# Kernel tuning notes

Measured on AMD Instinct MI355X. Metric: run time of the kernel, lower is better.

Reference implementation:

```python
import jax, jax.numpy as jnp
import numpy as np

N_EMBD = 1024
HEAD_SIZE = 64

def setup_inputs() -> dict:
    key = jax.random.key(0)
    kx, kk, kq, kv = jax.random.split(key, 4)
    x = jax.random.normal(kx, (8, 2048, N_EMBD), dtype=jnp.float32)
    # torch nn.Linear(n_embd, head_size, bias=False): y = x @ W.T, W:[head_size,n_embd].
    # We store the transposed form [n_embd, head_size] directly.
    s = 1.0 / np.sqrt(N_EMBD)
    Wk = jax.random.uniform(kk, (N_EMBD, HEAD_SIZE), jnp.float32, -s, s)
    Wq = jax.random.uniform(kq, (N_EMBD, HEAD_SIZE), jnp.float32, -s, s)
    Wv = jax.random.uniform(kv, (N_EMBD, HEAD_SIZE), jnp.float32, -s, s)
    return {"x": x, "Wk": Wk, "Wq": Wq, "Wv": Wv}

def reference(x, Wk, Wq, Wv):
    B, T, C = x.shape
    k = jnp.einsum('btc,cd->btd', x, Wk)  # [B,T,d]
    q = jnp.einsum('btc,cd->btd', x, Wq)
    v = jnp.einsum('btc,cd->btd', x, Wv)
    d = k.shape[-1]
    wei = jnp.einsum('btd,bsd->bts', q, k) * (d ** -0.5)  # [B,T,T]
    causal = jnp.tril(jnp.ones((T, T), dtype=bool))
    wei = jnp.where(causal, wei, -jnp.inf)
    wei = jax.nn.softmax(wei, axis=-1)
    # dropout p=0.0 -> identity (eval-mode equivalent)
    out = jnp.einsum('bts,bsd->btd', wei, v)  # [B,T,d]
    return out
```

## Files before the change

### kernel.cpp

```cpp
#include <hip/hip_runtime.h>
#include <hip/hip_bf16.h>

#define TB 8
#define TT 2048
#define TC 1024
#define TD 64
#define PSP 72

typedef __attribute__((ext_vector_type(8))) short bf16x8;
typedef __attribute__((ext_vector_type(4))) float f32x4;

__device__ __forceinline__ short f2bf(float f) {
    union { float f; unsigned u; } v; v.f = f;
    unsigned r = v.u + 0x7fffu + ((v.u >> 16) & 1u);
    return (short)(r >> 16);
}

__device__ __forceinline__ unsigned pk2(float a, float b) {
    __hip_bfloat162 h = __float22bfloat162_rn(make_float2(a, b));
    union { __hip_bfloat162 h2; unsigned u; } c; c.h2 = h;
    return c.u;
}

__device__ __forceinline__ void gl_lds16(const void* g, void* l) {
    __builtin_amdgcn_global_load_lds(
        (const __attribute__((address_space(1))) unsigned*)g,
        (__attribute__((address_space(3))) unsigned*)l, 16, 0, 0);
}

__device__ __forceinline__ void bar_raw() { asm volatile("s_barrier" ::: "memory"); }
#define WAIT_VM(n) asm volatile("s_waitcnt vmcnt(" #n ")" ::: "memory")

__global__ __launch_bounds__(256) void convert_w(const float* __restrict__ Wk,
                                                 const float* __restrict__ Wq,
                                                 const float* __restrict__ Wv,
                                                 short* __restrict__ Wt) {
    __shared__ short Tl[64 * PSP];
    const int tid = threadIdx.x;
    const int kc  = blockIdx.x;
    const int oid = blockIdx.y;
    const float* src = (oid == 0) ? Wk : (oid == 1) ? Wq : Wv;
    const float scale = (oid == 1) ? 0.125f : 1.0f;
    const int row = tid >> 2;
    const int c0  = (tid & 3) << 4;

    const float* sp = src + (size_t)(kc * 64 + row) * TD + c0;
    float4 a = ((const float4*)sp)[0], b = ((const float4*)sp)[1];
    float4 c = ((const float4*)sp)[2], d = ((const float4*)sp)[3];
    float vals[16] = {a.x,a.y,a.z,a.w, b.x,b.y,b.z,b.w,
                      c.x,c.y,c.z,c.w, d.x,d.y,d.z,d.w};
#pragma unroll
    for (int j = 0; j < 16; ++j)
        Tl[(c0 + j) * PSP + row] = f2bf(vals[j] * scale);
    __syncthreads();

    const int n  = tid >> 2;
    const int k0 = (tid & 3) << 4;
    uint4 u0 = *(uint4*)&Tl[n * PSP + k0];
    uint4 u1 = *(uint4*)&Tl[n * PSP + k0 + 8];
    uint4* dst = (uint4*)(Wt + (size_t)(oid * 64 + n) * TC + kc * 64 + k0);
    dst[0] = u0; dst[1] = u1;
}

__global__ __launch_bounds__(256, 1) void qkv_proj(const float* __restrict__ x,
                                                   const short* __restrict__ Wt,
                                                   short* __restrict__ qb,
                                                   short* __restrict__ kb,
                                                   short* __restrict__ vt) {
    __shared__ __align__(16) char sm[3 * 40960];
    const int tid = threadIdx.x;
    const int mg  = blockIdx.x;
    const int wv  = tid >> 6, lane = tid & 63;
    const int wu  = __builtin_amdgcn_readfirstlane(wv);
    const int l15 = lane & 15, quad = lane >> 4;
    const int mh  = wv >> 1;
    const int nh  = wv & 1;

    f32x4 acc[2][6];
#pragma unroll
    for (int i = 0; i < 2; ++i)
#pragma unroll
        for (int j = 0; j < 6; ++j) acc[i][j] = (f32x4){0.f, 0.f, 0.f, 0.f};

    const float* xtile = x + (size_t)mg * 64 * TC;

#define STAGE_Q(r)                                                          \
    {                                                                       \
        char* sb = sm + ((r) % 3) * 40960;                                  \
        float* xd = (float*)sb;                                             \
        short* wd = (short*)(sb + 16384);                                   \
        _Pragma("unroll")                                                   \
        for (int j = 0; j < 4; ++j) {                                       \
            int sbase = (j * 4 + wu) * 64;                                  \
            int sl = sbase + lane;                                          \
            int rw = sl >> 4, g = sl & 15;                                  \
            int gg = g ^ (rw & 15);                                         \
            gl_lds16(xtile + (size_t)rw * TC + (r) * 64 + gg * 4,           \
                     xd + (size_t)sbase * 4);                               \
        }                                                                   \
        _Pragma("unroll")                                                   \
        for (int j = 0; j < 6; ++j) {                                       \
            int n0 = (j * 4 + wu) * 8;                                      \
            int nb = n0 + (lane >> 3), g = lane & 7;                        \
            int gg = g ^ (nb & 7);                                          \
            gl_lds16(Wt + (size_t)nb * TC + (r) * 64 + gg * 8,              \
                     wd + (size_t)n0 * 64);                                 \
        }                                                                   \
    }

    STAGE_Q(0);
    STAGE_Q(1);
    for (int r = 0; r < 16; ++r) {
        if (r + 2 < 16)      { STAGE_Q(r + 2); WAIT_VM(20); }
        else if (r + 1 < 16) { WAIT_VM(10); }
        else                 { WAIT_VM(0); }
        bar_raw();
        const char* sb = sm + (r % 3) * 40960;
        const float* xb = (const float*)sb;
        const short* wb = (const short*)(sb + 16384);
#pragma unroll
        for (int c = 0; c < 2; ++c) {
            int G = c * 8 + quad * 2;
#pragma unroll
            for (int mt = 0; mt < 2; ++mt) {
                const int xrow = (mh * 32 + mt * 16 + l15) * 16;
                float4 f0 = *(const float4*)(xb + (xrow + (G ^ l15)) * 4);
                float4 f1 = *(const float4*)(xb + (xrow + ((G + 1) ^ l15)) * 4);
                union { bf16x8 v; unsigned u[4]; } pk;
                pk.u[0] = pk2(f0.x, f0.y); pk.u[1] = pk2(f0.z, f0.w);
                pk.u[2] = pk2(f1.x, f1.y); pk.u[3] = pk2(f1.z, f1.w);
#pragma unroll
                for (int i = 0; i < 6; ++i) {
                    int nt = nh * 6 + i;
                    bf16x8 B = *(const bf16x8*)(wb + (nt * 16 + l15) * 64
                                                + (((c * 4 + quad) ^ (l15 & 7)) * 8));
                    acc[mt][i] = __builtin_amdgcn_mfma_f32_16x16x32_bf16(
                                     pk.v, B, acc[mt][i], 0, 0, 0);
                }
            }
        }
        bar_raw();
    }
#undef STAGE_Q

    const int row0 = mg * 64 + mh * 32;
    const int bb = mg >> 5;
#pragma unroll
    for (int i = 0; i < 6; ++i) {
        int nt = nh * 6 + i;
        if (nt < 4) {
#pragma unroll
            for (int mt = 0; mt < 2; ++mt)
#pragma unroll
                for (int rr = 0; rr < 4; ++rr)
                    kb[(size_t)(row0 + mt * 16 + quad * 4 + rr) * TD + nt * 16 + l15]
                        = f2bf(acc[mt][rr >> 2 ? 0 : i][rr]);
        }
    }
#pragma unroll
    for (int i = 0; i < 6; ++i) {
        int nt = nh * 6 + i;
#pragma unroll
        for (int mt = 0; mt < 2; ++mt) {
            if (nt < 4) {
#pragma unroll
                for (int rr = 0; rr < 4; ++rr)
                    kb[(size_t)(row0 + mt * 16 + quad * 4 + rr) * TD + nt * 16 + l15]
                        = f2bf(acc[mt][i][rr]);
            } else if (nt < 8) {
#pragma unroll
                for (int rr = 0; rr < 4; ++rr)
                    qb[(size_t)(row0 + mt * 16 + quad * 4 + rr) * TD + (nt - 4) * 16 + l15]
                        = f2bf(acc[mt][i][rr]);
            } else {
                int d = (nt - 8) * 16 + l15;
                alignas(8) short t4[4];
#pragma unroll
                for (int rr = 0; rr < 4; ++rr) t4[rr] = f2bf(acc[mt][i][rr]);
                *(uint2*)(vt + (size_t)(bb * TD + d) * TT
                          + ((row0 + mt * 16) & 2047) + quad * 4) = *(uint2*)t4;
            }
        }
    }
}

__global__ __launch_bounds__(256, 2) void attn(const short* __restrict__ qb,
                                               const short* __restrict__ kb,
                                               const short* __restrict__ vt,
                                               float* __restrict__ out) {
    __shared__ __align__(16) char smem[58368];
    short* Ps = (short*)(smem + 49152);

    const int tid = threadIdx.x;
    const int pm  = blockIdx.x;
    const int b   = pm & 7;
    const int it  = 31 - (pm >> 3);
    const int wv  = tid >> 6, lane = tid & 63;
    const int wu  = __builtin_amdgcn_readfirstlane(wv);
    const int l15 = lane & 15, quad = lane >> 4;
    const int q0  = it * 64;
    const int KT  = it + 1;
    const float L2E = 1.4426950408889634f;

    const short* kbb = kb + (size_t)b * TT * TD;
    const short* vbb = vt + (size_t)b * TD * TT;
    short* myPs = Ps + wu * (16 * PSP);

    const size_t qoff = (size_t)(b * TT + q0 + wv * 16 + l15) * TD + quad * 8;
    bf16x8 aq0 = *(const bf16x8*)(qb + qoff);
    bf16x8 aq1 = *(const bf16x8*)(qb + qoff + 32);
    WAIT_VM(0);

    f32x4 O[4];
#pragma unroll
    for (int i = 0; i < 4; ++i) O[i] = (f32x4){0.f, 0.f, 0.f, 0.f};
    float lsum[4] = {0.f, 0.f, 0.f, 0.f};

#define STAGE_KV(r)                                                         \
    {                                                                       \
        char* sb = smem + ((r) % 3) * 16384;                                \
        short* kd = (short*)sb;                                             \
        short* vd = (short*)(sb + 8192);                                    \
        _Pragma("unroll")                                                   \
        for (int j = 0; j < 2; ++j) {                                       \
            int sbase = (j * 4 + wu) * 64;                                  \
            int sl = sbase + lane;                                          \
            int rw = sl >> 3, g = sl & 7;                                   \
            int gg = g ^ (rw & 7);                                          \
            gl_lds16(kbb + (size_t)((r) * 64 + rw) * TD + gg * 8,           \
                     kd + sbase * 8);                                       \
            gl_lds16(vbb + (size_t)rw * TT + (r) * 64 + gg * 8,             \
                     vd + sbase * 8);                                       \
        }                                                                   \
    }

    STAGE_KV(0);
    if (KT > 1) STAGE_KV(1);
    for (int r = 0; r < KT; ++r) {
        if (r + 2 < KT)      { STAGE_KV(r + 2); WAIT_VM(8); }
        else if (r + 1 < KT) { WAIT_VM(4); }
        else                 { WAIT_VM(0); }
        bar_raw();

        const char* sb2 = (const char*)smem + (r % 3) * 16384;
        const short* Kt = (const short*)sb2;
        const short* Vt = (const short*)(sb2 + 8192);
        f32x4 S[4];
#pragma unroll
        for (int nt = 0; nt < 4; ++nt) {
            int rw = nt * 16 + l15, r7 = l15 & 7;
            bf16x8 b0 = *(const bf16x8*)(Kt + rw * 64 + (quad ^ r7) * 8);
            bf16x8 b1 = *(const bf16x8*)(Kt + rw * 64 + ((4 + quad) ^ r7) * 8);
            S[nt] = (f32x4){0.f, 0.f, 0.f, 0.f};
            S[nt] = __builtin_amdgcn_mfma_f32_16x16x32_bf16(aq0, b0, S[nt], 0, 0, 0);
            S[nt] = __builtin_amdgcn_mfma_f32_16x16x32_bf16(aq1, b1, S[nt], 0, 0, 0);
        }
        const bool diag = (r == KT - 1);
        const int qrow = q0 + wv * 16 + quad * 4;
#pragma unroll
        for (int nt = 0; nt < 4; ++nt) {
            int scol = r * 64 + nt * 16 + l15;
#pragma unroll
            for (int r4 = 0; r4 < 4; ++r4) {
                float pv = exp2f(S[nt][r4] * L2E);
                if (diag && (scol > qrow + r4)) pv = 0.f;
                lsum[r4] += pv;
                myPs[(quad * 4 + r4) * PSP + nt * 16 + l15] = f2bf(pv);
            }
        }
        bf16x8 p0 = *(const bf16x8*)(myPs + l15 * PSP + quad * 8);
        bf16x8 p1 = *(const bf16x8*)(myPs + l15 * PSP + quad * 8 + 32);
#pragma unroll
        for (int dt = 0; dt < 4; ++dt) {
            int rw = dt * 16 + l15, r7 = l15 & 7;
            bf16x8 b0 = *(const bf16x8*)(Vt + rw * 64 + (quad ^ r7) * 8);
            bf16x8 b1 = *(const bf16x8*)(Vt + rw * 64 + ((4 + quad) ^ r7) * 8);
            O[dt] = __builtin_amdgcn_mfma_f32_16x16x32_bf16(p0, b0, O[dt], 0, 0, 0);
            O[dt] = __builtin_amdgcn_mfma_f32_16x16x32_bf16(p1, b1, O[dt], 0, 0, 0);
        }
        bar_raw();
    }
#undef STAGE_KV

#pragma unroll
    for (int r4 = 0; r4 < 4; ++r4) {
        float v = lsum[r4];
        v += __shfl_xor(v, 1); v += __shfl_xor(v, 2);
        v += __shfl_xor(v, 4); v += __shfl_xor(v, 8);
        lsum[r4] = v;
    }
#pragma unroll
    for (int dt = 0; dt < 4; ++dt)
#pragma unroll
        for (int r4 = 0; r4 < 4; ++r4)
            out[(size_t)(b * TT + q0 + wv * 16 + quad * 4 + r4) * TD + dt * 16 + l15]
                = O[dt][r4] / lsum[r4];
}

extern "C" void kernel_launch(void* const* d_in, const int* in_sizes, int n_in,
                              void* d_out, int out_size, void* d_ws, size_t ws_size,
                              hipStream_t stream) {
    const float* x  = (const float*)d_in[0];
    const float* Wk = (const float*)d_in[1];
    const float* Wq = (const float*)d_in[2];
    const float* Wv = (const float*)d_in[3];
    float* out = (float*)d_out;

    char* ws = (char*)d_ws;
    short* Wt = (short*)(ws);
    short* qb = (short*)(ws + 524288);
    short* kb = (short*)(ws + 2621440);
    short* vt = (short*)(ws + 4718592);

    convert_w<<<dim3(16, 3), dim3(256), 0, stream>>>(Wk, Wq, Wv, Wt);
    qkv_proj<<<dim3(256), dim3(256), 0, stream>>>(x, Wt, qb, kb, vt);
    attn<<<dim3(256), dim3(256), 0, stream>>>(qb, kb, vt, out);
}
```

Measured before the change: 143.8 us.

## Halve qkv_proj row tile for more blocks; make attn waves own 32 query rows

The projection kernel now handles 32 rows per block instead of 64. It launches 512 blocks, uses double buffering instead of triple, and lowers shared memory so two blocks can share a CU. The attention kernel moves from 4 waves with 16 query rows each to 2 waves with 32 rows each. Each wave now reuses its K/V fragments loaded from LDS across two M-tiles, which cuts LDS reads per MFMA. The trade-offs are more register pressure in attn, fewer waves per block to hide latency, and a shallower prefetch pipeline in qkv_proj.

```diff
diff --git a/kernel.cpp b/kernel.cpp
--- a/kernel.cpp
+++ b/kernel.cpp
@@ -62,12 +62,12 @@
     dst[0] = u0; dst[1] = u1;
 }
 
-__global__ __launch_bounds__(256, 1) void qkv_proj(const float* __restrict__ x,
+__global__ __launch_bounds__(256, 2) void qkv_proj(const float* __restrict__ x,
                                                    const short* __restrict__ Wt,
                                                    short* __restrict__ qb,
                                                    short* __restrict__ kb,
                                                    short* __restrict__ vt) {
-    __shared__ __align__(16) char sm[3 * 40960];
+    __shared__ __align__(16) char sm[2 * 32768];
     const int tid = threadIdx.x;
     const int mg  = blockIdx.x;
     const int wv  = tid >> 6, lane = tid & 63;
@@ -76,21 +76,19 @@
     const int mh  = wv >> 1;
     const int nh  = wv & 1;
 
-    f32x4 acc[2][6];
-#pragma unroll
-    for (int i = 0; i < 2; ++i)
-#pragma unroll
-        for (int j = 0; j < 6; ++j) acc[i][j] = (f32x4){0.f, 0.f, 0.f, 0.f};
-
-    const float* xtile = x + (size_t)mg * 64 * TC;
+    f32x4 acc[6];
+#pragma unroll
+    for (int j = 0; j < 6; ++j) acc[j] = (f32x4){0.f, 0.f, 0.f, 0.f};
+
+    const float* xtile = x + (size_t)mg * 32 * TC;
 
 #define STAGE_Q(r)                                                          \
     {                                                                       \
-        char* sb = sm + ((r) % 3) * 40960;                                  \
+        char* sb = sm + ((r) & 1) * 32768;                                  \
         float* xd = (float*)sb;                                             \
-        short* wd = (short*)(sb + 16384);                                   \
+        short* wd = (short*)(sb + 8192);                                    \
         _Pragma("unroll")                                                   \
-        for (int j = 0; j < 4; ++j) {                                       \
+        for (int j = 0; j < 2; ++j) {                                       \
             int sbase = (j * 4 + wu) * 64;                                  \
             int sl = sbase + lane;                                          \
             int rw = sl >> 4, g = sl & 15;                                  \
@@ -109,82 +107,61 @@
     }
 
     STAGE_Q(0);
-    STAGE_Q(1);
     for (int r = 0; r < 16; ++r) {
-        if (r + 2 < 16)      { STAGE_Q(r + 2); WAIT_VM(20); }
-        else if (r + 1 < 16) { WAIT_VM(10); }
-        else                 { WAIT_VM(0); }
+        if (r + 1 < 16) { STAGE_Q(r + 1); WAIT_VM(8); }
+        else            { WAIT_VM(0); }
         bar_raw();
-        const char* sb = sm + (r % 3) * 40960;
+        const char* sb = sm + (r & 1) * 32768;
         const float* xb = (const float*)sb;
-        const short* wb = (const short*)(sb + 16384);
+        const short* wb = (const short*)(sb + 8192);
+        const int xrow = (mh * 16 + l15) * 16;
 #pragma unroll
         for (int c = 0; c < 2; ++c) {
             int G = c * 8 + quad * 2;
-#pragma unroll
-            for (int mt = 0; mt < 2; ++mt) {
-                const int xrow = (mh * 32 + mt * 16 + l15) * 16;
-                float4 f0 = *(const float4*)(xb + (xrow + (G ^ l15)) * 4);
-                float4 f1 = *(const float4*)(xb + (xrow + ((G + 1) ^ l15)) * 4);
-                union { bf16x8 v; unsigned u[4]; } pk;
-                pk.u[0] = pk2(f0.x, f0.y); pk.u[1] = pk2(f0.z, f0.w);
-                pk.u[2] = pk2(f1.x, f1.y); pk.u[3] = pk2(f1.z, f1.w);
-#pragma unroll
-                for (int i = 0; i < 6; ++i) {
-                    int nt = nh * 6 + i;
-                    bf16x8 B = *(const bf16x8*)(wb + (nt * 16 + l15) * 64
-                                                + (((c * 4 + quad) ^ (l15 & 7)) * 8));
-                    acc[mt][i] = __builtin_amdgcn_mfma_f32_16x16x32_bf16(
-                                     pk.v, B, acc[mt][i], 0, 0, 0);
-                }
+            float4 f0 = *(const float4*)(xb + (xrow + (G ^ l15)) * 4);
+            float4 f1 = *(const float4*)(xb + (xrow + ((G + 1) ^ l15)) * 4);
+            union { bf16x8 v; unsigned u[4]; } pk;
+            pk.u[0] = pk2(f0.x, f0.y); pk.u[1] = pk2(f0.z, f0.w);
+            pk.u[2] = pk2(f1.x, f1.y); pk.u[3] = pk2(f1.z, f1.w);
+#pragma unroll
+            for (int i = 0; i < 6; ++i) {
+                int nt = nh * 6 + i;
+                bf16x8 B = *(const bf16x8*)(wb + (nt * 16 + l15) * 64
+                                            + (((c * 4 + quad) ^ (l15 & 7)) * 8));
+                acc[i] = __builtin_amdgcn_mfma_f32_16x16x32_bf16(pk.v, B, acc[i], 0, 0, 0);
             }
         }
         bar_raw();
     }
 #undef STAGE_Q
 
-    const int row0 = mg * 64 + mh * 32;
-    const int bb = mg >> 5;
+    const int row0 = mg * 32 + mh * 16;
+    const int bb = mg >> 6;
 #pragma unroll
     for (int i = 0; i < 6; ++i) {
         int nt = nh * 6 + i;
         if (nt < 4) {
 #pragma unroll
-            for (int mt = 0; mt < 2; ++mt)
-#pragma unroll
-                for (int rr = 0; rr < 4; ++rr)
-                    kb[(size_t)(row0 + mt * 16 + quad * 4 + rr) * TD + nt * 16 + l15]
-                        = f2bf(acc[mt][rr >> 2 ? 0 : i][rr]);
-        }
-    }
-#pragma unroll
-    for (int i = 0; i < 6; ++i) {
-        int nt = nh * 6 + i;
-#pragma unroll
-        for (int mt = 0; mt < 2; ++mt) {
-            if (nt < 4) {
-#pragma unroll
-                for (int rr = 0; rr < 4; ++rr)
-                    kb[(size_t)(row0 + mt * 16 + quad * 4 + rr) * TD + nt * 16 + l15]
-                        = f2bf(acc[mt][i][rr]);
-            } else if (nt < 8) {
-#pragma unroll
-                for (int rr = 0; rr < 4; ++rr)
-                    qb[(size_t)(row0 + mt * 16 + quad * 4 + rr) * TD + (nt - 4) * 16 + l15]
-                        = f2bf(acc[mt][i][rr]);
-            } else {
-                int d = (nt - 8) * 16 + l15;
-                alignas(8) short t4[4];
-#pragma unroll
-                for (int rr = 0; rr < 4; ++rr) t4[rr] = f2bf(acc[mt][i][rr]);
-                *(uint2*)(vt + (size_t)(bb * TD + d) * TT
-                          + ((row0 + mt * 16) & 2047) + quad * 4) = *(uint2*)t4;
-            }
-        }
-    }
-}
-
-__global__ __launch_bounds__(256, 2) void attn(const short* __restrict__ qb,
+            for (int rr = 0; rr < 4; ++rr)
+                kb[(size_t)(row0 + quad * 4 + rr) * TD + nt * 16 + l15]
+                    = f2bf(acc[i][rr]);
+        } else if (nt < 8) {
+#pragma unroll
+            for (int rr = 0; rr < 4; ++rr)
+                qb[(size_t)(row0 + quad * 4 + rr) * TD + (nt - 4) * 16 + l15]
+                    = f2bf(acc[i][rr]);
+        } else {
+            int d = (nt - 8) * 16 + l15;
+            alignas(8) short t4[4];
+#pragma unroll
+            for (int rr = 0; rr < 4; ++rr) t4[rr] = f2bf(acc[i][rr]);
+            *(uint2*)(vt + (size_t)(bb * TD + d) * TT
+                      + (row0 & 2047) + quad * 4) = *(uint2*)t4;
+        }
+    }
+}
+
+__global__ __launch_bounds__(128, 2) void attn(const short* __restrict__ qb,
                                                const short* __restrict__ kb,
                                                const short* __restrict__ vt,
                                                float* __restrict__ out) {
@@ -204,17 +181,23 @@
 
     const short* kbb = kb + (size_t)b * TT * TD;
     const short* vbb = vt + (size_t)b * TD * TT;
-    short* myPs = Ps + wu * (16 * PSP);
-
-    const size_t qoff = (size_t)(b * TT + q0 + wv * 16 + l15) * TD + quad * 8;
-    bf16x8 aq0 = *(const bf16x8*)(qb + qoff);
-    bf16x8 aq1 = *(const bf16x8*)(qb + qoff + 32);
+    short* myPs = Ps + wu * (32 * PSP);
+
+    bf16x8 aq[2][2];
+#pragma unroll
+    for (int mt = 0; mt < 2; ++mt) {
+        const size_t qoff = (size_t)(b * TT + q0 + wv * 32 + mt * 16 + l15) * TD + quad * 8;
+        aq[mt][0] = *(const bf16x8*)(qb + qoff);
+        aq[mt][1] = *(const bf16x8*)(qb + qoff + 32);
+    }
     WAIT_VM(0);
 
-    f32x4 O[4];
-#pragma unroll
-    for (int i = 0; i < 4; ++i) O[i] = (f32x4){0.f, 0.f, 0.f, 0.f};
-    float lsum[4] = {0.f, 0.f, 0.f, 0.f};
+    f32x4 O[2][4];
+#pragma unroll
+    for (int mt = 0; mt < 2; ++mt)
+#pragma unroll
+        for (int i = 0; i < 4; ++i) O[mt][i] = (f32x4){0.f, 0.f, 0.f, 0.f};
+    float lsum[2][4] = {{0.f,0.f,0.f,0.f},{0.f,0.f,0.f,0.f}};
 
 #define STAGE_KV(r)                                                         \
     {                                                                       \
@@ -222,8 +205,8 @@
         short* kd = (short*)sb;                                             \
         short* vd = (short*)(sb + 8192);                                    \
         _Pragma("unroll")                                                   \
-        for (int j = 0; j < 2; ++j) {                                       \
-            int sbase = (j * 4 + wu) * 64;                                  \
+        for (int j = 0; j < 4; ++j) {                                       \
+            int sbase = (j * 2 + wu) * 64;                                  \
             int sl = sbase + lane;                                          \
             int rw = sl >> 3, g = sl & 7;                                   \
             int gg = g ^ (rw & 7);                                          \
@@ -237,64 +220,82 @@
     STAGE_KV(0);
     if (KT > 1) STAGE_KV(1);
     for (int r = 0; r < KT; ++r) {
-        if (r + 2 < KT)      { STAGE_KV(r + 2); WAIT_VM(8); }
-        else if (r + 1 < KT) { WAIT_VM(4); }
+        if (r + 2 < KT)      { STAGE_KV(r + 2); WAIT_VM(16); }
+        else if (r + 1 < KT) { WAIT_VM(8); }
         else                 { WAIT_VM(0); }
         bar_raw();
 
         const char* sb2 = (const char*)smem + (r % 3) * 16384;
         const short* Kt = (const short*)sb2;
         const short* Vt = (const short*)(sb2 + 8192);
-        f32x4 S[4];
+
+        bf16x8 kf[4][2];
 #pragma unroll
         for (int nt = 0; nt < 4; ++nt) {
             int rw = nt * 16 + l15, r7 = l15 & 7;
-            bf16x8 b0 = *(const bf16x8*)(Kt + rw * 64 + (quad ^ r7) * 8);
-            bf16x8 b1 = *(const bf16x8*)(Kt + rw * 64 + ((4 + quad) ^ r7) * 8);
-            S[nt] = (f32x4){0.f, 0.f, 0.f, 0.f};
-            S[nt] = __builtin_amdgcn_mfma_f32_16x16x32_bf16(aq0, b0, S[nt], 0, 0, 0);
-            S[nt] = __builtin_amdgcn_mfma_f32_16x16x32_bf16(aq1, b1, S[nt], 0, 0, 0);
+            kf[nt][0] = *(const bf16x8*)(Kt + rw * 64 + (quad ^ r7) * 8);
+            kf[nt][1] = *(const bf16x8*)(Kt + rw * 64 + ((4 + quad) ^ r7) * 8);
         }
         const bool diag = (r == KT - 1);
-        const int qrow = q0 + wv * 16 + quad * 4;
-#pragma unroll
-        for (int nt = 0; nt < 4; ++nt) {
-            int scol = r * 64 + nt * 16 + l15;
-#pragma unroll
-            for (int r4 = 0; r4 < 4; ++r4) {
-                float pv = exp2f(S[nt][r4] * L2E);
-                if (diag && (scol > qrow + r4)) pv = 0.f;
-                lsum[r4] += pv;
-                myPs[(quad * 4 + r4) * PSP + nt * 16 + l15] = f2bf(pv);
+#pragma unroll
+        for (int mt = 0; mt < 2; ++mt) {
+            f32x4 S[4];
+#pragma unroll
+            for (int nt = 0; nt < 4; ++nt) {
+                S[nt] = (f32x4){0.f, 0.f, 0.f, 0.f};
+                S[nt] = __builtin_amdgcn_mfma_f32_16x16x32_bf16(aq[mt][0], kf[nt][0], S[nt], 0, 0, 0);
+                S[nt] = __builtin_amdgcn_mfma_f32_16x16x32_bf16(aq[mt][1], kf[nt][1], S[nt], 0, 0, 0);
             }
-        }
-        bf16x8 p0 = *(const bf16x8*)(myPs + l15 * PSP + quad * 8);
-        bf16x8 p1 = *(const bf16x8*)(myPs + l15 * PSP + quad * 8 + 32);
+            const int qrow = q0 + wv * 32 + mt * 16 + quad * 4;
+#pragma unroll
+            for (int nt = 0; nt < 4; ++nt) {
+                int scol = r * 64 + nt * 16 + l15;
+#pragma unroll
+                for (int r4 = 0; r4 < 4; ++r4) {
+                    float pv = exp2f(S[nt][r4] * L2E);
+                    if (diag && (scol > qrow + r4)) pv = 0.f;
+                    lsum[mt][r4] += pv;
+                    myPs[(mt * 16 + quad * 4 + r4) * PSP + nt * 16 + l15] = f2bf(pv);
+                }
+            }
+        }
+        bf16x8 vf[4][2];
 #pragma unroll
         for (int dt = 0; dt < 4; ++dt) {
             int rw = dt * 16 + l15, r7 = l15 & 7;
-            bf16x8 b0 = *(const bf16x8*)(Vt + rw * 64 + (quad ^ r7) * 8);
-            bf16x8 b1 = *(const bf16x8*)(Vt + rw * 64 + ((4 + quad) ^ r7) * 8);
-            O[dt] = __builtin_amdgcn_mfma_f32_16x16x32_bf16(p0, b0, O[dt], 0, 0, 0);
-            O[dt] = __builtin_amdgcn_mfma_f32_16x16x32_bf16(p1, b1, O[dt], 0, 0, 0);
+            vf[dt][0] = *(const bf16x8*)(Vt + rw * 64 + (quad ^ r7) * 8);
+            vf[dt][1] = *(const bf16x8*)(Vt + rw * 64 + ((4 + quad) ^ r7) * 8);
+        }
+#pragma unroll
+        for (int mt = 0; mt < 2; ++mt) {
+            bf16x8 p0 = *(const bf16x8*)(myPs + (mt * 16 + l15) * PSP + quad * 8);
+            bf16x8 p1 = *(const bf16x8*)(myPs + (mt * 16 + l15) * PSP + quad * 8 + 32);
+#pragma unroll
+            for (int dt = 0; dt < 4; ++dt) {
+                O[mt][dt] = __builtin_amdgcn_mfma_f32_16x16x32_bf16(p0, vf[dt][0], O[mt][dt], 0, 0, 0);
+                O[mt][dt] = __builtin_amdgcn_mfma_f32_16x16x32_bf16(p1, vf[dt][1], O[mt][dt], 0, 0, 0);
+            }
         }
         bar_raw();
     }
 #undef STAGE_KV
 
 #pragma unroll
-    for (int r4 = 0; r4 < 4; ++r4) {
-        float v = lsum[r4];
-        v += __shfl_xor(v, 1); v += __shfl_xor(v, 2);
-        v += __shfl_xor(v, 4); v += __shfl_xor(v, 8);
-        lsum[r4] = v;
-    }
-#pragma unroll
-    for (int dt = 0; dt < 4; ++dt)
-#pragma unroll
-        for (int r4 = 0; r4 < 4; ++r4)
-            out[(size_t)(b * TT + q0 + wv * 16 + quad * 4 + r4) * TD + dt * 16 + l15]
-                = O[dt][r4] / lsum[r4];
+    for (int mt = 0; mt < 2; ++mt) {
+#pragma unroll
+        for (int r4 = 0; r4 < 4; ++r4) {
+            float v = lsum[mt][r4];
+            v += __shfl_xor(v, 1); v += __shfl_xor(v, 2);
+            v += __shfl_xor(v, 4); v += __shfl_xor(v, 8);
+            lsum[mt][r4] = v;
+        }
+#pragma unroll
+        for (int dt = 0; dt < 4; ++dt)
+#pragma unroll
+            for (int r4 = 0; r4 < 4; ++r4)
+                out[(size_t)(b * TT + q0 + wv * 32 + mt * 16 + quad * 4 + r4) * TD
+                    + dt * 16 + l15] = O[mt][dt][r4] / lsum[mt][r4];
+    }
 }
 
 extern "C" void kernel_launch(void* const* d_in, const int* in_sizes, int n_in,
@@ -313,6 +314,6 @@
     short* vt = (short*)(ws + 4718592);
 
     convert_w<<<dim3(16, 3), dim3(256), 0, stream>>>(Wk, Wq, Wv, Wt);
-    qkv_proj<<<dim3(256), dim3(256), 0, stream>>>(x, Wt, qb, kb, vt);
-    attn<<<dim3(256), dim3(256), 0, stream>>>(qb, kb, vt, out);
-}
+    qkv_proj<<<dim3(512), dim3(256), 0, stream>>>(x, Wt, qb, kb, vt);
+    attn<<<dim3(256), dim3(128), 0, stream>>>(qb, kb, vt, out);
+}
```

After: 162.2 us. 1.13x slower.
